# Kernel optimization log

Hardware: AMD Instinct MI355X
Metric: run time of the kernel (lower is better)

Reference implementation:

```python
import jax, jax.numpy as jnp
import numpy as np

HIDDEN = 2048
N_HEADS = 16
N_KV_GROUPS = 4
HEAD_DIM = HIDDEN // N_HEADS  # 128
LATENT = 512
KV_SIZE = HIDDEN * N_KV_GROUPS // N_HEADS  # 512


def setup_inputs() -> dict:
    key = jax.random.key(0)
    ks = jax.random.split(key, 11)
    s = 0.02
    return {
        "hidden_states": jax.random.normal(ks[0], (2, 2048, HIDDEN), dtype=jnp.float32),
        "Wq": jax.random.normal(ks[1], (HIDDEN, HIDDEN), dtype=jnp.float32) * s,
        "bq": jnp.zeros((HIDDEN,), dtype=jnp.float32),
        "Wl": jax.random.normal(ks[2], (HIDDEN, LATENT), dtype=jnp.float32) * s,
        "bl": jnp.zeros((LATENT,), dtype=jnp.float32),
        "Wk": jax.random.normal(ks[3], (LATENT, KV_SIZE), dtype=jnp.float32) * s,
        "bk": jnp.zeros((KV_SIZE,), dtype=jnp.float32),
        "Wv": jax.random.normal(ks[4], (LATENT, KV_SIZE), dtype=jnp.float32) * s,
        "bv": jnp.zeros((KV_SIZE,), dtype=jnp.float32),
        "Wo": jax.random.normal(ks[5], (HIDDEN, HIDDEN), dtype=jnp.float32) * s,
        "bo": jnp.zeros((HIDDEN,), dtype=jnp.float32),
    }


def reference(hidden_states, Wq, bq, Wl, bl, Wk, bk, Wv, bv, Wo, bo):
    B, S, _ = hidden_states.shape
    heads_per_group = N_HEADS // N_KV_GROUPS

    q = hidden_states @ Wq + bq                      # [B,S,H*D]
    latent = hidden_states @ Wl + bl                 # [B,S,L]
    k = latent @ Wk + bk                             # [B,S,G*D]
    v = latent @ Wv + bv

    q = q.reshape(B, S, N_HEADS, HEAD_DIM).transpose(0, 2, 1, 3)        # [B,H,S,D]
    k = k.reshape(B, S, N_KV_GROUPS, HEAD_DIM).transpose(0, 2, 1, 3)    # [B,G,S,D]
    v = v.reshape(B, S, N_KV_GROUPS, HEAD_DIM).transpose(0, 2, 1, 3)

    # repeat_interleave over head dim: group g -> heads [g*hpg, (g+1)*hpg)
    k = jnp.repeat(k, heads_per_group, axis=1)       # [B,H,S,D]
    v = jnp.repeat(v, heads_per_group, axis=1)

    scale = 1.0 / np.sqrt(HEAD_DIM).astype(np.float32)
    scores = jnp.einsum("bhqd,bhkd->bhqk", q, k) * scale
    probs = jax.nn.softmax(scores, axis=-1)          # dropout p=0 (eval) -> identity
    ctx = jnp.einsum("bhqk,bhkd->bhqd", probs, v)    # [B,H,S,D]
    ctx = ctx.transpose(0, 2, 1, 3).reshape(B, S, HIDDEN)
    return ctx @ Wo + bo
```

## Files before the change

### kernel.cpp

```cpp
#include <hip/hip_runtime.h>
#include <stdint.h>


#define DEV static __device__ __forceinline__

using short8 = __attribute__((ext_vector_type(8))) short;
using f32x4  = __attribute__((ext_vector_type(4))) float;

typedef __attribute__((address_space(1))) void gvoid;
typedef __attribute__((address_space(3))) void lvoid;

DEV unsigned short f2b(float f) {
  unsigned u = __builtin_bit_cast(unsigned, f);
  unsigned r = (u + 0x7fffu + ((u >> 16) & 1u)) >> 16;
  return (unsigned short)r;
}
DEV float b2f(unsigned short s) {
  unsigned u = ((unsigned)s) << 16;
  return __builtin_bit_cast(float, u);
}
DEV float as_f32(float v) { return v; }
DEV float as_f32(unsigned short v) { return b2f(v); }

DEV unsigned pack2bf(float lo, float hi) {
  return (unsigned)f2b(lo) | ((unsigned)f2b(hi) << 16);
}

DEV unsigned cvtpk(float lo, float hi) {
  unsigned r;
  asm("v_cvt_pk_bf16_f32 %0, %1, %2" : "=v"(r) : "v"(lo), "v"(hi));
  return r;
}

DEV float ex2(float x) { return __builtin_amdgcn_exp2f(x); }

DEV void async16(const void* g, void* l) {
  __builtin_amdgcn_global_load_lds((gvoid*)(uintptr_t)g,
                                   (lvoid*)(uint32_t)(uintptr_t)l, 16, 0, 0);
}

DEV f32x4 mfma16(short8 a, short8 b, f32x4 c) {
  return __builtin_amdgcn_mfma_f32_16x16x32_bf16(a, b, c, 0, 0, 0);
}

__global__ __launch_bounds__(256) void cvt_f32_bf16(
    const float* __restrict__ in, unsigned short* __restrict__ out, long n) {
  long i = ((long)blockIdx.x * 256 + threadIdx.x) * 8;
  if (i >= n) return;
  float4 a = *(const float4*)(in + i);
  float4 b = *(const float4*)(in + i + 4);
  short8 o;
  o[0] = (short)f2b(a.x); o[1] = (short)f2b(a.y);
  o[2] = (short)f2b(a.z); o[3] = (short)f2b(a.w);
  o[4] = (short)f2b(b.x); o[5] = (short)f2b(b.y);
  o[6] = (short)f2b(b.z); o[7] = (short)f2b(b.w);
  *(short8*)(out + i) = o;
}

template <typename TIN>
__global__ __launch_bounds__(256) void transpose_to_bf16(
    const TIN* __restrict__ in, unsigned short* __restrict__ out, int R, int C) {
  __shared__ float tile[32][33];
  size_t batch = (size_t)blockIdx.z * (size_t)R * C;
  int bc = blockIdx.x * 32, br = blockIdx.y * 32;
  int tx = threadIdx.x & 31, ty0 = threadIdx.x >> 5;
#pragma unroll
  for (int ty = ty0; ty < 32; ty += 8)
    tile[ty][tx] = as_f32(in[batch + (size_t)(br + ty) * C + bc + tx]);
  __syncthreads();
#pragma unroll
  for (int ty = ty0; ty < 32; ty += 8)
    out[batch + (size_t)(bc + ty) * R + br + tx] = f2b(tile[tx][ty]);
}

__global__ __launch_bounds__(256) void transpose_v(
    const unsigned short* __restrict__ in, unsigned short* __restrict__ out) {
  __shared__ float tile[32][33];
  int b = blockIdx.z;
  int bc = blockIdx.x * 32;
  int br = blockIdx.y * 32;
  const unsigned short* ip = in + (size_t)b * 2048 * 1024 + 512;
  unsigned short* op = out + (size_t)b * 512 * 2048;
  int tx = threadIdx.x & 31, ty0 = threadIdx.x >> 5;
#pragma unroll
  for (int ty = ty0; ty < 32; ty += 8)
    tile[ty][tx] = b2f(ip[(size_t)(br + ty) * 1024 + bc + tx]);
  __syncthreads();
#pragma unroll
  for (int ty = ty0; ty < 32; ty += 8)
    op[(size_t)(bc + ty) * 2048 + br + tx] = f2b(tile[tx][ty]);
}

template <int OUT_F32>
__global__ __launch_bounds__(256) void gemm_bt(
    const unsigned short* __restrict__ A, const unsigned short* __restrict__ Bt,
    const float* __restrict__ bias, void* __restrict__ Cout,
    int M, int N, int K, float scale) {
  __shared__ unsigned short As[128 * 32];
  __shared__ unsigned short Bs[128 * 32];
  int tid = threadIdx.x;
  int lane = tid & 63, wave = tid >> 6;
  int wr = wave >> 1, wc = wave & 1;
  int lq = lane & 15, grp = lane >> 4;
  int brow = blockIdx.y * 128, bcol = blockIdx.x * 128;

  f32x4 acc[4][4] = {};

  for (int k0 = 0; k0 < K; k0 += 32) {
    {
      int e0 = tid * 8;
      int r0 = e0 >> 5, c0 = e0 & 31;
      async16(A + (size_t)(brow + r0) * K + k0 + c0, As + e0);
      async16(Bt + (size_t)(bcol + r0) * K + k0 + c0, Bs + e0);
      int e1 = (256 + tid) * 8;
      int r1 = e1 >> 5, c1 = e1 & 31;
      async16(A + (size_t)(brow + r1) * K + k0 + c1, As + e1);
      async16(Bt + (size_t)(bcol + r1) * K + k0 + c1, Bs + e1);
    }
    __syncthreads();

    short8 af[4], bf[4];
#pragma unroll
    for (int m = 0; m < 4; m++)
      af[m] = *(const short8*)(As + (wr * 64 + m * 16 + lq) * 32 + grp * 8);
#pragma unroll
    for (int n = 0; n < 4; n++)
      bf[n] = *(const short8*)(Bs + (wc * 64 + n * 16 + lq) * 32 + grp * 8);
#pragma unroll
    for (int m = 0; m < 4; m++)
#pragma unroll
      for (int n = 0; n < 4; n++)
        acc[m][n] = mfma16(af[m], bf[n], acc[m][n]);
    __syncthreads();
  }

#pragma unroll
  for (int n = 0; n < 4; n++) {
    int col = bcol + wc * 64 + n * 16 + lq;
    float bv = bias[col];
#pragma unroll
    for (int m = 0; m < 4; m++) {
#pragma unroll
      for (int r = 0; r < 4; r++) {
        int row = brow + wr * 64 + m * 16 + grp * 4 + r;
        float v = (acc[m][n][r] + bv) * scale;
        if (OUT_F32)
          ((float*)Cout)[(size_t)row * N + col] = v;
        else
          ((unsigned short*)Cout)[(size_t)row * N + col] = f2b(v);
      }
    }
  }
}

template <int OUT_F32>
__global__ __launch_bounds__(512, 2) void gemm_bt_256(
    const unsigned short* __restrict__ A, const unsigned short* __restrict__ Bt,
    const float* __restrict__ bias, void* __restrict__ Cout,
    int M, int N, int K, float scale) {
  __shared__ __align__(1024) unsigned short As[2][16384];
  __shared__ __align__(1024) unsigned short Bs[2][8192];
  const int tid = threadIdx.x;
  const int lane = tid & 63, wave = tid >> 6;
  const int wr = wave >> 1, wc = wave & 1;
  const int lq = lane & 15, grp = lane >> 4;

  const int gx = gridDim.x;
  int nwg = gx * gridDim.y;
  int bid = blockIdx.y * gx + blockIdx.x;
  int wgid = (bid & 7) * (nwg >> 3) + (bid >> 3);
  int bx = wgid % gx, by = wgid / gx;
  const int brow = by * 256, bcol = bx * 128;

#define MKSLOT(db, mat, rb)                                            \
  ({ int d_ = (db) + lane * 16;                                        \
     int L_ = d_ ^ (((d_ >> 9) & 1) << 5);                             \
     (mat) + (size_t)((rb) + (L_ >> 7)) * K + ((L_ & 127) >> 1); })
  const int dbA0 = wave * 1024, dbA1 = dbA0 + 8192, dbA2 = dbA0 + 16384,
            dbA3 = dbA0 + 24576;
  const int dbB0 = (wave < 4) ? wave * 1024 : 8192 + (wave - 4) * 1024;
  const int dbB1 = dbB0 + 4096;
  const unsigned short* srcA0 = MKSLOT(dbA0, A, brow);
  const unsigned short* srcA1 = MKSLOT(dbA1, A, brow);
  const unsigned short* srcA2 = MKSLOT(dbA2, A, brow);
  const unsigned short* srcA3 = MKSLOT(dbA3, A, brow);
  const unsigned short* srcB0 = MKSLOT(dbB0, Bt, bcol);
  const unsigned short* srcB1 = MKSLOT(dbB1, Bt, bcol);
  char* dstA0 = (char*)&As[0][0] + dbA0 + lane * 16;
  char* dstA1 = (char*)&As[0][0] + dbA1 + lane * 16;
  char* dstA2 = (char*)&As[0][0] + dbA2 + lane * 16;
  char* dstA3 = (char*)&As[0][0] + dbA3 + lane * 16;
  char* dstB0 = (char*)&Bs[0][0] + dbB0 + lane * 16;
  char* dstB1 = (char*)&Bs[0][0] + dbB1 + lane * 16;
#define STA(i, b, k0) async16(srcA##i + (k0), dstA##i + (b) * 32768)
#define STB(i, b, k0) async16(srcB##i + (k0), dstB##i + (b) * 16384)

  auto ldA = [&](int cur, int row, int kk) -> short8 {
    int p = row * 128 + kk * 64 + grp * 16;
    p ^= ((p >> 9) & 1) << 5;
    return *(const short8*)((const char*)&As[cur][0] + p);
  };
  auto ldB = [&](int cur, int row, int kk) -> short8 {
    int p = row * 128 + kk * 64 + grp * 16;
    p ^= ((p >> 9) & 1) << 5;
    return *(const short8*)((const char*)&Bs[cur][0] + p);
  };

  f32x4 acc[4][4] = {};
  short8 af[4][2], bf[4][2];
  const int NT = K >> 6;

  STA(0, 0, 0); STA(1, 0, 0); STA(2, 0, 0); STA(3, 0, 0);
  STB(0, 0, 0); STB(1, 0, 0);
  asm volatile("s_waitcnt vmcnt(1)" ::: "memory");
  __builtin_amdgcn_s_barrier();

  for (int t = 0; t < NT; ++t) {
    const int cur = t & 1, nb = cur ^ 1;
    const bool pf = (t + 1 < NT);
    const int k0n = (t + 1) << 6;

#pragma unroll
    for (int m = 0; m < 4; m++) {
      af[m][0] = ldA(cur, wr * 64 + m * 16 + lq, 0);
      af[m][1] = ldA(cur, wr * 64 + m * 16 + lq, 1);
    }
#pragma unroll
    for (int n = 0; n < 2; n++) {
      bf[n][0] = ldB(cur, wc * 64 + n * 16 + lq, 0);
      bf[n][1] = ldB(cur, wc * 64 + n * 16 + lq, 1);
    }
    if (pf) { STA(0, nb, k0n); STA(1, nb, k0n); STA(2, nb, k0n); }
    __builtin_amdgcn_s_barrier();
    __builtin_amdgcn_s_setprio(1);
#pragma unroll
    for (int m = 0; m < 4; m++)
#pragma unroll
      for (int n = 0; n < 2; n++) {
        acc[m][n] = mfma16(af[m][0], bf[n][0], acc[m][n]);
        acc[m][n] = mfma16(af[m][1], bf[n][1], acc[m][n]);
      }
    __builtin_amdgcn_s_setprio(0);
    __builtin_amdgcn_s_barrier();

    if (pf) {
      STA(3, nb, k0n); STB(0, nb, k0n); STB(1, nb, k0n);
      asm volatile("s_waitcnt vmcnt(6)" ::: "memory");
    } else {
      asm volatile("s_waitcnt vmcnt(0)" ::: "memory");
    }
    __builtin_amdgcn_s_barrier();
#pragma unroll
    for (int n = 0; n < 2; n++) {
      bf[2 + n][0] = ldB(cur, wc * 64 + (2 + n) * 16 + lq, 0);
      bf[2 + n][1] = ldB(cur, wc * 64 + (2 + n) * 16 + lq, 1);
    }
    __builtin_amdgcn_s_setprio(1);
#pragma unroll
    for (int m = 0; m < 4; m++)
#pragma unroll
      for (int n = 2; n < 4; n++) {
        acc[m][n] = mfma16(af[m][0], bf[n][0], acc[m][n]);
        acc[m][n] = mfma16(af[m][1], bf[n][1], acc[m][n]);
      }
    __builtin_amdgcn_s_setprio(0);
    if (pf) {
      asm volatile("s_waitcnt vmcnt(1)" ::: "memory");
    }
    __builtin_amdgcn_s_barrier();
  }

#pragma unroll
  for (int n = 0; n < 4; n++) {
    int col = bcol + wc * 64 + n * 16 + lq;
    float bv = bias[col];
#pragma unroll
    for (int m = 0; m < 4; m++) {
#pragma unroll
      for (int r = 0; r < 4; r++) {
        int row = brow + wr * 64 + m * 16 + grp * 4 + r;
        float v = (acc[m][n][r] + bv) * scale;
        if (OUT_F32)
          ((float*)Cout)[(size_t)row * N + col] = v;
        else
          ((unsigned short*)Cout)[(size_t)row * N + col] = f2b(v);
      }
    }
  }
#undef STA
#undef STB
#undef MKSLOT
}

__global__ __launch_bounds__(256, 2) void attn_kernel(
    const unsigned short* __restrict__ q,
    const unsigned short* __restrict__ kv,
    const unsigned short* __restrict__ vt,
    unsigned short* __restrict__ ctx) {
  __shared__ unsigned short KV[2][32][512];
  const int lane = threadIdx.x & 63, wave = threadIdx.x >> 6;
  const int lq = lane & 15, grp = lane >> 4;
  const int bid = blockIdx.x;
  const int combo = bid & 7;
  const int slot = bid >> 3;
  const int b = combo >> 2, g = combo & 3;
  const int h = g * 4 + (slot >> 4);
  const int qbase = (slot & 15) * 128 + wave * 32;

  short8 qf[2][4];
#pragma unroll
  for (int qs = 0; qs < 2; qs++) {
    const unsigned short* qp =
        q + ((size_t)(b * 2048 + qbase + qs * 16 + lq)) * 2048 + h * 128 + grp * 8;
#pragma unroll
    for (int c = 0; c < 4; c++) qf[qs][c] = *(const short8*)(qp + c * 32);
  }

  f32x4 o[2][8] = {};
  float lsum[2] = {0.f, 0.f};
  const float C = 20.0f;

  const int kvperm = (lq >> 2) * 8 + (lq & 3);
  const unsigned short* kB = kv + (size_t)b * 2048 * 1024 + g * 128 + grp * 8;
  const unsigned short* vB =
      vt + ((size_t)((b * 4 + g) * 128 + lq)) * 2048 + grp * 8;
  const int fbase = wave * 8;
  unsigned short* dstb = &KV[0][fbase][0] + lane * 8;

  auto stage = [&](int bn, int kv0) {
    unsigned short* dst = dstb + bn * 16384;
    if (fbase < 16) {
#pragma unroll
      for (int j = 0; j < 8; j++) {
        int f = fbase + j, t = f >> 2, c = f & 3;
        const unsigned short* src =
            kB + (size_t)(kv0 + (t >> 1) * 32 + (t & 1) * 4 + kvperm) * 1024 + c * 32;
        async16(src, dst + j * 512);
      }
    } else {
#pragma unroll
      for (int j = 0; j < 8; j++) {
        int f = fbase - 16 + j, d0 = f >> 1, u = f & 1;
        const unsigned short* src = vB + (size_t)(d0 * 16) * 2048 + kv0 + u * 32;
        async16(src, dst + j * 512);
      }
    }
  };

  stage(0, 0);
  int buf = 0;
  for (int it = 0; it < 32; ++it) {
    __syncthreads();
    if (it < 31) stage(buf ^ 1, (it + 1) * 64);
    const unsigned short* Kb = &KV[buf][0][0] + lane * 8;

    f32x4 s[2][4] = {};
    __builtin_amdgcn_s_setprio(1);
#pragma unroll
    for (int c = 0; c < 4; c++) {
      short8 kf0 = *(const short8*)(Kb + (0 + c) * 512);
      short8 kf1 = *(const short8*)(Kb + (4 + c) * 512);
      short8 kf2 = *(const short8*)(Kb + (8 + c) * 512);
      short8 kf3 = *(const short8*)(Kb + (12 + c) * 512);
#pragma unroll
      for (int qs = 0; qs < 2; qs++) {
        s[qs][0] = mfma16(kf0, qf[qs][c], s[qs][0]);
        s[qs][1] = mfma16(kf1, qf[qs][c], s[qs][1]);
        s[qs][2] = mfma16(kf2, qf[qs][c], s[qs][2]);
        s[qs][3] = mfma16(kf3, qf[qs][c], s[qs][3]);
      }
    }
    __builtin_amdgcn_s_setprio(0);

    short8 pf[2][2];
#pragma unroll
    for (int qs = 0; qs < 2; qs++) {
      float ps = 0.f;
      union { short8 v; unsigned w[4]; } pk0, pk1;
#pragma unroll
      for (int t = 0; t < 4; t++) {
        float e0 = ex2(s[qs][t][0] - C);
        float e1 = ex2(s[qs][t][1] - C);
        float e2 = ex2(s[qs][t][2] - C);
        float e3 = ex2(s[qs][t][3] - C);
        ps += (e0 + e1) + (e2 + e3);
        unsigned w0 = cvtpk(e0, e1), w1 = cvtpk(e2, e3);
        if (t == 0) { pk0.w[0] = w0; pk0.w[1] = w1; }
        else if (t == 1) { pk0.w[2] = w0; pk0.w[3] = w1; }
        else if (t == 2) { pk1.w[0] = w0; pk1.w[1] = w1; }
        else { pk1.w[2] = w0; pk1.w[3] = w1; }
      }
      lsum[qs] += ps;
      pf[qs][0] = pk0.v;
      pf[qs][1] = pk1.v;
    }

    const unsigned short* Vb = Kb + 16 * 512;
    __builtin_amdgcn_s_setprio(1);
#pragma unroll
    for (int d0 = 0; d0 < 8; d0++) {
      short8 v0 = *(const short8*)(Vb + (d0 * 2 + 0) * 512);
      short8 v1 = *(const short8*)(Vb + (d0 * 2 + 1) * 512);
#pragma unroll
      for (int qs = 0; qs < 2; qs++) {
        o[qs][d0] = mfma16(pf[qs][0], v0, o[qs][d0]);
        o[qs][d0] = mfma16(pf[qs][1], v1, o[qs][d0]);
      }
    }
    __builtin_amdgcn_s_setprio(0);
    buf ^= 1;
  }

  unsigned short* cp = ctx + ((size_t)(b * 2048 + qbase)) * 2048 + h * 128;
#pragma unroll
  for (int qs = 0; qs < 2; qs++) {
    float l = lsum[qs];
    l += __shfl_xor(l, 16);
    l += __shfl_xor(l, 32);
    float ri = 1.0f / l;
    float r0 = __shfl(ri, grp * 4 + 0), r1 = __shfl(ri, grp * 4 + 1);
    float r2 = __shfl(ri, grp * 4 + 2), r3 = __shfl(ri, grp * 4 + 3);
#pragma unroll
    for (int d0 = 0; d0 < 8; d0++) {
      int col = d0 * 16 + lq;
      cp[(size_t)(qs * 16 + grp * 4 + 0) * 2048 + col] = f2b(o[qs][d0][0] * r0);
      cp[(size_t)(qs * 16 + grp * 4 + 1) * 2048 + col] = f2b(o[qs][d0][1] * r1);
      cp[(size_t)(qs * 16 + grp * 4 + 2) * 2048 + col] = f2b(o[qs][d0][2] * r2);
      cp[(size_t)(qs * 16 + grp * 4 + 3) * 2048 + col] = f2b(o[qs][d0][3] * r3);
    }
  }
}

extern "C" void kernel_launch(void* const* d_in, const int* in_sizes, int n_in,
                              void* d_out, int out_size, void* d_ws, size_t ws_size,
                              hipStream_t stream) {
  const float* h  = (const float*)d_in[0];
  const float* Wq = (const float*)d_in[1];
  const float* bq = (const float*)d_in[2];
  const float* Wl = (const float*)d_in[3];
  const float* bl = (const float*)d_in[4];
  const float* Wk = (const float*)d_in[5];
  const float* bk = (const float*)d_in[6];
  const float* Wv = (const float*)d_in[7];
  const float* bv = (const float*)d_in[8];
  const float* Wo = (const float*)d_in[9];
  const float* bo = (const float*)d_in[10];
  float* out = (float*)d_out;

  const int M = 4096;

  char* w = (char*)d_ws;
  auto take = [&](size_t elems) {
    void* p = (void*)w;
    w += (elems * 2 + 255) & ~(size_t)255;
    return (unsigned short*)p;
  };
  unsigned short* hb   = take(8388608);
  unsigned short* WqT  = take(4194304);
  unsigned short* WlT  = take(1048576);
  unsigned short* WkvT = take(524288);
  unsigned short* WoT  = take(4194304);
  unsigned short* qb   = take(8388608);
  unsigned short* lat  = take(2097152);
  unsigned short* kvb  = take(4194304);
  unsigned short* vtb  = take(2097152);
  unsigned short* ctx  = take(8388608);
  float* bkv = (float*)take(2048);

  cvt_f32_bf16<<<4096, 256, 0, stream>>>(h, hb, 8388608L);
  transpose_to_bf16<float><<<dim3(64, 64, 1), 256, 0, stream>>>(Wq, WqT, 2048, 2048);
  transpose_to_bf16<float><<<dim3(16, 64, 1), 256, 0, stream>>>(Wl, WlT, 2048, 512);
  transpose_to_bf16<float><<<dim3(16, 16, 1), 256, 0, stream>>>(Wk, WkvT, 512, 512);
  transpose_to_bf16<float><<<dim3(16, 16, 1), 256, 0, stream>>>(Wv, WkvT + 262144, 512, 512);
  transpose_to_bf16<float><<<dim3(64, 64, 1), 256, 0, stream>>>(Wo, WoT, 2048, 2048);
  (void)hipMemcpyAsync(bkv, bk, 512 * sizeof(float), hipMemcpyDeviceToDevice, stream);
  (void)hipMemcpyAsync(bkv + 512, bv, 512 * sizeof(float), hipMemcpyDeviceToDevice, stream);

  const float scale = 0.08838834764831845f * 1.4426950408889634f;
  gemm_bt_256<0><<<dim3(16, 16), 512, 0, stream>>>(hb, WqT, bq, qb, M, 2048, 2048, scale);
  gemm_bt<0><<<dim3(4, 32), 256, 0, stream>>>(hb, WlT, bl, lat, M, 512, 2048, 1.0f);
  gemm_bt<0><<<dim3(8, 32), 256, 0, stream>>>(lat, WkvT, bkv, kvb, M, 1024, 512, 1.0f);

  transpose_v<<<dim3(16, 64, 2), 256, 0, stream>>>(kvb, vtb);

  attn_kernel<<<512, 256, 0, stream>>>(qb, kvb, vtb, ctx);

  gemm_bt_256<1><<<dim3(16, 16), 512, 0, stream>>>(ctx, WoT, bo, out, M, 2048, 2048, 1.0f);
}
```

Measured before the change: 259.6 us.

## Fuse prep kernels into one launch and merge Q and latent GEMMs

Replaces the separate conversion, transpose and bias-copy launches with a single mega_prep kernel that dispatches on block index. It also concatenates Wq and Wl into one weight so the Q and latent projections run as a single wider GEMM that writes a combined buffer. The softmax scale is folded into Wq and bq at prep time. The K/V GEMM and attention read that combined buffer through a strided leading dimension. This cuts launch overhead and one GEMM launch, at the cost of a strided A read and a wider output layout.

```diff
diff --git a/kernel.cpp b/kernel.cpp
--- a/kernel.cpp
+++ b/kernel.cpp
@@ -19,12 +19,6 @@
   unsigned u = ((unsigned)s) << 16;
   return __builtin_bit_cast(float, u);
 }
-DEV float as_f32(float v) { return v; }
-DEV float as_f32(unsigned short v) { return b2f(v); }
-
-DEV unsigned pack2bf(float lo, float hi) {
-  return (unsigned)f2b(lo) | ((unsigned)f2b(hi) << 16);
-}
 
 DEV unsigned cvtpk(float lo, float hi) {
   unsigned r;
@@ -43,34 +37,66 @@
   return __builtin_amdgcn_mfma_f32_16x16x32_bf16(a, b, c, 0, 0, 0);
 }
 
-__global__ __launch_bounds__(256) void cvt_f32_bf16(
-    const float* __restrict__ in, unsigned short* __restrict__ out, long n) {
-  long i = ((long)blockIdx.x * 256 + threadIdx.x) * 8;
-  if (i >= n) return;
-  float4 a = *(const float4*)(in + i);
-  float4 b = *(const float4*)(in + i + 4);
-  short8 o;
-  o[0] = (short)f2b(a.x); o[1] = (short)f2b(a.y);
-  o[2] = (short)f2b(a.z); o[3] = (short)f2b(a.w);
-  o[4] = (short)f2b(b.x); o[5] = (short)f2b(b.y);
-  o[6] = (short)f2b(b.z); o[7] = (short)f2b(b.w);
-  *(short8*)(out + i) = o;
-}
-
-template <typename TIN>
-__global__ __launch_bounds__(256) void transpose_to_bf16(
-    const TIN* __restrict__ in, unsigned short* __restrict__ out, int R, int C) {
+__global__ __launch_bounds__(256) void mega_prep(
+    const float* __restrict__ h, unsigned short* __restrict__ hb,
+    const float* __restrict__ Wq, const float* __restrict__ Wl,
+    const float* __restrict__ Wk, const float* __restrict__ Wv,
+    const float* __restrict__ Wo,
+    unsigned short* __restrict__ WqlT, unsigned short* __restrict__ WkvT,
+    unsigned short* __restrict__ WoT,
+    const float* __restrict__ bq, const float* __restrict__ bl,
+    const float* __restrict__ bk, const float* __restrict__ bv,
+    float* __restrict__ bql, float* __restrict__ bkv, float qscale) {
   __shared__ float tile[32][33];
-  size_t batch = (size_t)blockIdx.z * (size_t)R * C;
-  int bc = blockIdx.x * 32, br = blockIdx.y * 32;
-  int tx = threadIdx.x & 31, ty0 = threadIdx.x >> 5;
+  const int bid = blockIdx.x;
+  const int tid = threadIdx.x;
+
+  if (bid < 4096) {
+    long i = ((long)bid * 256 + tid) * 8;
+    float4 a = *(const float4*)(h + i);
+    float4 b = *(const float4*)(h + i + 4);
+    short8 o;
+    o[0] = (short)f2b(a.x); o[1] = (short)f2b(a.y);
+    o[2] = (short)f2b(a.z); o[3] = (short)f2b(a.w);
+    o[4] = (short)f2b(b.x); o[5] = (short)f2b(b.y);
+    o[6] = (short)f2b(b.z); o[7] = (short)f2b(b.w);
+    *(short8*)(hb + i) = o;
+    return;
+  }
+
+  const float* in; unsigned short* out; int R, C, bx, by; float sc = 1.0f;
+  if (bid < 8192) {
+    int l = bid - 4096; in = Wq; out = WqlT; R = 2048; C = 2048;
+    bx = l & 63; by = l >> 6; sc = qscale;
+  } else if (bid < 9216) {
+    int l = bid - 8192; in = Wl; out = WqlT + 2048 * 2048; R = 2048; C = 512;
+    bx = l & 15; by = l >> 4;
+  } else if (bid < 9472) {
+    int l = bid - 9216; in = Wk; out = WkvT; R = 512; C = 512;
+    bx = l & 15; by = l >> 4;
+  } else if (bid < 9728) {
+    int l = bid - 9472; in = Wv; out = WkvT + 262144; R = 512; C = 512;
+    bx = l & 15; by = l >> 4;
+  } else if (bid < 13824) {
+    int l = bid - 9728; in = Wo; out = WoT; R = 2048; C = 2048;
+    bx = l & 63; by = l >> 6;
+  } else {
+    for (int t = tid; t < 2560; t += 256)
+      bql[t] = (t < 2048) ? bq[t] * qscale : bl[t - 2048];
+    for (int t = tid; t < 1024; t += 256)
+      bkv[t] = (t < 512) ? bk[t] : bv[t - 512];
+    return;
+  }
+
+  int bc = bx * 32, br = by * 32;
+  int tx = tid & 31, ty0 = tid >> 5;
 #pragma unroll
   for (int ty = ty0; ty < 32; ty += 8)
-    tile[ty][tx] = as_f32(in[batch + (size_t)(br + ty) * C + bc + tx]);
+    tile[ty][tx] = in[(size_t)(br + ty) * C + bc + tx] * sc;
   __syncthreads();
 #pragma unroll
   for (int ty = ty0; ty < 32; ty += 8)
-    out[batch + (size_t)(bc + ty) * R + br + tx] = f2b(tile[tx][ty]);
+    out[(size_t)(bc + ty) * R + br + tx] = f2b(tile[tx][ty]);
 }
 
 __global__ __launch_bounds__(256) void transpose_v(
@@ -95,7 +121,7 @@
 __global__ __launch_bounds__(256) void gemm_bt(
     const unsigned short* __restrict__ A, const unsigned short* __restrict__ Bt,
     const float* __restrict__ bias, void* __restrict__ Cout,
-    int M, int N, int K, float scale) {
+    int M, int N, int K, int lda, float scale) {
   __shared__ unsigned short As[128 * 32];
   __shared__ unsigned short Bs[128 * 32];
   int tid = threadIdx.x;
@@ -110,11 +136,11 @@
     {
       int e0 = tid * 8;
       int r0 = e0 >> 5, c0 = e0 & 31;
-      async16(A + (size_t)(brow + r0) * K + k0 + c0, As + e0);
+      async16(A + (size_t)(brow + r0) * lda + k0 + c0, As + e0);
       async16(Bt + (size_t)(bcol + r0) * K + k0 + c0, Bs + e0);
       int e1 = (256 + tid) * 8;
       int r1 = e1 >> 5, c1 = e1 & 31;
-      async16(A + (size_t)(brow + r1) * K + k0 + c1, As + e1);
+      async16(A + (size_t)(brow + r1) * lda + k0 + c1, As + e1);
       async16(Bt + (size_t)(bcol + r1) * K + k0 + c1, Bs + e1);
     }
     __syncthreads();
@@ -311,7 +337,7 @@
 #pragma unroll
   for (int qs = 0; qs < 2; qs++) {
     const unsigned short* qp =
-        q + ((size_t)(b * 2048 + qbase + qs * 16 + lq)) * 2048 + h * 128 + grp * 8;
+        q + ((size_t)(b * 2048 + qbase + qs * 16 + lq)) * 2560 + h * 128 + grp * 8;
 #pragma unroll
     for (int c = 0; c < 4; c++) qf[qs][c] = *(const short8*)(qp + c * 32);
   }
@@ -456,34 +482,28 @@
     return (unsigned short*)p;
   };
   unsigned short* hb   = take(8388608);
-  unsigned short* WqT  = take(4194304);
-  unsigned short* WlT  = take(1048576);
+  unsigned short* WqlT = take(5242880);
   unsigned short* WkvT = take(524288);
   unsigned short* WoT  = take(4194304);
-  unsigned short* qb   = take(8388608);
-  unsigned short* lat  = take(2097152);
+  unsigned short* qlat = take(10485760);
   unsigned short* kvb  = take(4194304);
   unsigned short* vtb  = take(2097152);
   unsigned short* ctx  = take(8388608);
-  float* bkv = (float*)take(2048);
-
-  cvt_f32_bf16<<<4096, 256, 0, stream>>>(h, hb, 8388608L);
-  transpose_to_bf16<float><<<dim3(64, 64, 1), 256, 0, stream>>>(Wq, WqT, 2048, 2048);
-  transpose_to_bf16<float><<<dim3(16, 64, 1), 256, 0, stream>>>(Wl, WlT, 2048, 512);
-  transpose_to_bf16<float><<<dim3(16, 16, 1), 256, 0, stream>>>(Wk, WkvT, 512, 512);
-  transpose_to_bf16<float><<<dim3(16, 16, 1), 256, 0, stream>>>(Wv, WkvT + 262144, 512, 512);
-  transpose_to_bf16<float><<<dim3(64, 64, 1), 256, 0, stream>>>(Wo, WoT, 2048, 2048);
-  (void)hipMemcpyAsync(bkv, bk, 512 * sizeof(float), hipMemcpyDeviceToDevice, stream);
-  (void)hipMemcpyAsync(bkv + 512, bv, 512 * sizeof(float), hipMemcpyDeviceToDevice, stream);
+  float* bql = (float*)take(2560);
+  float* bkv = (float*)take(1024);
 
   const float scale = 0.08838834764831845f * 1.4426950408889634f;
-  gemm_bt_256<0><<<dim3(16, 16), 512, 0, stream>>>(hb, WqT, bq, qb, M, 2048, 2048, scale);
-  gemm_bt<0><<<dim3(4, 32), 256, 0, stream>>>(hb, WlT, bl, lat, M, 512, 2048, 1.0f);
-  gemm_bt<0><<<dim3(8, 32), 256, 0, stream>>>(lat, WkvT, bkv, kvb, M, 1024, 512, 1.0f);
+
+  mega_prep<<<13825, 256, 0, stream>>>(h, hb, Wq, Wl, Wk, Wv, Wo,
+                                       WqlT, WkvT, WoT,
+                                       bq, bl, bk, bv, bql, bkv, scale);
+
+  gemm_bt_256<0><<<dim3(20, 16), 512, 0, stream>>>(hb, WqlT, bql, qlat, M, 2560, 2048, 1.0f);
+  gemm_bt<0><<<dim3(8, 32), 256, 0, stream>>>(qlat + 2048, WkvT, bkv, kvb, M, 1024, 512, 2560, 1.0f);
 
   transpose_v<<<dim3(16, 64, 2), 256, 0, stream>>>(kvb, vtb);
 
-  attn_kernel<<<512, 256, 0, stream>>>(qb, kvb, vtb, ctx);
+  attn_kernel<<<512, 256, 0, stream>>>(qlat, kvb, vtb, ctx);
 
   gemm_bt_256<1><<<dim3(16, 16), 512, 0, stream>>>(ctx, WoT, bo, out, M, 2048, 2048, 1.0f);
 }
```

Result: faster. 244.2 us (-5.9%).
